# Kernel optimization log

Measured on AMD Instinct MI355X. Metric: run time of the kernel, lower is better.

The kernel has to match this reference:

```python
import jax, jax.numpy as jnp
import numpy as np

B, N, D, H = 16, 256, 1024, 8
DK = D // H
WAVE_LEN = 1000.0


def box_relational_embedding(boxes):
    # boxes: (B, N, 4) as (x_min, y_min, x_max, y_max)
    x_min, y_min, x_max, y_max = jnp.split(boxes, 4, axis=-1)  # each (B, N, 1)
    cx = (x_min + x_max) * 0.5
    cy = (y_min + y_max) * 0.5
    w = (x_max - x_min) + 1.0
    h = (y_max - y_min) + 1.0
    # pairwise deltas (B, N, N); row i = query box, col j = key box
    delta_x = jnp.log(jnp.clip(jnp.abs((cx - jnp.swapaxes(cx, -2, -1)) / w), 1e-3, None))
    delta_y = jnp.log(jnp.clip(jnp.abs((cy - jnp.swapaxes(cy, -2, -1)) / h), 1e-3, None))
    delta_w = jnp.log(w / jnp.swapaxes(w, -2, -1))
    delta_h = jnp.log(h / jnp.swapaxes(h, -2, -1))
    pos = jnp.stack([delta_x, delta_y, delta_w, delta_h], axis=-1)  # (B, N, N, 4)
    # sinusoidal expansion: dim_g = 64 -> 8 frequencies per delta
    feat_range = jnp.arange(8, dtype=pos.dtype) / 8.0
    dim_mat = 1.0 / (WAVE_LEN ** feat_range)  # (8,)
    mul = (100.0 * pos)[..., None] * dim_mat  # (B, N, N, 4, 8)
    mul = mul.reshape(pos.shape[:3] + (32,))
    return jnp.concatenate([jnp.sin(mul), jnp.cos(mul)], axis=-1)  # (B, N, N, 64)


def setup_inputs() -> dict:
    key = jax.random.key(0)
    ks = jax.random.split(key, 12)
    x = jax.random.normal(ks[0], (B, N, D), dtype=jnp.float32)
    # valid boxes: x_max > x_min, y_max > y_min
    xy = jax.random.uniform(ks[1], (B, N, 2), dtype=jnp.float32) * 100.0
    wh = jax.random.uniform(ks[2], (B, N, 2), dtype=jnp.float32) * 50.0 + 1.0
    boxes = jnp.concatenate([xy, xy + wh], axis=-1)
    s = 1.0 / np.sqrt(D)
    Wq = jax.random.normal(ks[3], (D, D), dtype=jnp.float32) * s
    Wk = jax.random.normal(ks[4], (D, D), dtype=jnp.float32) * s
    Wv = jax.random.normal(ks[5], (D, D), dtype=jnp.float32) * s
    Wo = jax.random.normal(ks[6], (D, D), dtype=jnp.float32) * s
    bq = jnp.zeros((D,), jnp.float32)
    bk = jnp.zeros((D,), jnp.float32)
    bv = jnp.zeros((D,), jnp.float32)
    bo = jnp.zeros((D,), jnp.float32)
    Wg = jax.random.normal(ks[7], (H, 64), dtype=jnp.float32) * (1.0 / 8.0)  # 8 per-head (64->1) linears
    bg = jnp.zeros((H,), jnp.float32)
    return {"x": x, "boxes": boxes, "Wq": Wq, "bq": bq, "Wk": Wk, "bk": bk,
            "Wv": Wv, "bv": bv, "Wo": Wo, "bo": bo, "Wg": Wg, "bg": bg}


def reference(x, boxes, Wq, bq, Wk, bk, Wv, bv, Wo, bo, Wg, bg):
    emb = box_relational_embedding(boxes)  # (B, N, N, 64)
    # per-head geometric weights, ReLU'd: (B, H, N, N)
    geo = jax.nn.relu(jnp.einsum('bnmg,hg->bhnm', emb, Wg) + bg[None, :, None, None])
    q = (x @ Wq + bq).reshape(B, N, H, DK).transpose(0, 2, 1, 3)  # (B, H, N, DK)
    k = (x @ Wk + bk).reshape(B, N, H, DK).transpose(0, 2, 1, 3)
    v = (x @ Wv + bv).reshape(B, N, H, DK).transpose(0, 2, 1, 3)
    scores = jnp.einsum('bhnd,bhmd->bhnm', q, k) / np.sqrt(DK)
    w_mn = jax.nn.softmax(jnp.log(jnp.clip(geo, 1e-6, None)) + scores, axis=-1)
    out = jnp.einsum('bhnm,bhmd->bhnd', w_mn, v)  # (B, H, N, DK)
    out = out.transpose(0, 2, 1, 3).reshape(B, N, D)
    return out @ Wo + bo
```

## Files before the change

kernel.cpp:

```cpp
#include <hip/hip_runtime.h>
#include <hip/hip_fp16.h>

#define Bb 16
#define Nn 256
#define Dd 1024
#define Hh 8
#define DKk 128

typedef unsigned short u16;
typedef __attribute__((ext_vector_type(8))) short bfrag;
typedef __attribute__((ext_vector_type(4))) float f4;

#define MFMA16(a, b, c) __builtin_amdgcn_mfma_f32_16x16x32_bf16((a), (b), (c), 0, 0, 0)

__device__ __forceinline__ u16 f2b(float f) {
  unsigned int u = __builtin_bit_cast(unsigned int, f);
  u += 0x7fffu + ((u >> 16) & 1u);
  return (u16)(u >> 16);
}

typedef __attribute__((address_space(1))) void GV;
typedef __attribute__((address_space(3))) void LV;
__device__ __forceinline__ void gload16(const void* g, void* l) {
  __builtin_amdgcn_global_load_lds((GV*)g, (LV*)l, 16, 0, 0);
}

__global__ __launch_bounds__(256) void cast_x_kernel(const float* __restrict__ x,
                                                     u16* __restrict__ xb) {
  const int i = blockIdx.x * 256 + threadIdx.x;
  const float4 v = ((const float4*)x)[i];
  union { u16 u[4]; unsigned long long ll; } p;
  p.u[0] = f2b(v.x); p.u[1] = f2b(v.y); p.u[2] = f2b(v.z); p.u[3] = f2b(v.w);
  ((unsigned long long*)xb)[i] = p.ll;
}

__global__ __launch_bounds__(256) void transpose_w_kernel(
    const float* __restrict__ Wq, const float* __restrict__ Wk,
    const float* __restrict__ Wv, const float* __restrict__ Wo,
    u16* __restrict__ wqkvt, u16* __restrict__ wot) {
  __shared__ float t[32][33];
  const int bid = blockIdx.x;
  const int which = bid >> 10;
  const int tr = (bid >> 5) & 31;
  const int tc = bid & 31;
  const float* W = which == 0 ? Wq : which == 1 ? Wk : which == 2 ? Wv : Wo;
  u16* dst = (which == 3) ? wot : (wqkvt + (long long)which * 1024 * 1024);
  const int tx = threadIdx.x & 31, ty = threadIdx.x >> 5;
#pragma unroll
  for (int rr = 0; rr < 4; rr++)
    t[ty + rr * 8][tx] = W[(tr * 32 + ty + rr * 8) * 1024 + tc * 32 + tx];
  __syncthreads();
#pragma unroll
  for (int rr = 0; rr < 4; rr++)
    dst[(tc * 32 + ty + rr * 8) * 1024 + tr * 32 + tx] = f2b(t[tx][ty + rr * 8]);
}

__global__ __launch_bounds__(256) void transpose_v_kernel(const u16* __restrict__ v,
                                                          u16* __restrict__ vT) {
  __shared__ u16 t[32][33];
  const int bid = blockIdx.x;
  const int bh = bid >> 5;
  const int kt = (bid >> 2) & 7;
  const int ct = bid & 3;
  const u16* src = v + (long long)bh * Nn * DKk;
  u16* dst = vT + (long long)bh * DKk * Nn;
  const int tx = threadIdx.x & 31, ty = threadIdx.x >> 5;
#pragma unroll
  for (int rr = 0; rr < 4; rr++)
    t[ty + rr * 8][tx] = src[(kt * 32 + ty + rr * 8) * DKk + ct * 32 + tx];
  __syncthreads();
#pragma unroll
  for (int rr = 0; rr < 4; rr++)
    dst[(ct * 32 + ty + rr * 8) * Nn + kt * 32 + tx] = t[tx][ty + rr * 8];
}

__global__ __launch_bounds__(256) void geo_kernel(const float* __restrict__ boxes,
                                                  const float* __restrict__ Wg,
                                                  const float* __restrict__ bg,
                                                  __half* __restrict__ logg) {
  __shared__ float wg_s[512];
  __shared__ float bg_s[8];
  const int tid = threadIdx.x;
  wg_s[tid] = Wg[tid];
  wg_s[tid + 256] = Wg[tid + 256];
  if (tid < 8) bg_s[tid] = bg[tid];
  __syncthreads();
  const int bid = blockIdx.x;
  const int b = bid >> 8, i = bid & 255;
  const int j = tid;
  const float4 bi4 = ((const float4*)boxes)[b * 256 + i];
  const float4 bj4 = ((const float4*)boxes)[b * 256 + j];
  const float cxi = (bi4.x + bi4.z) * 0.5f, cyi = (bi4.y + bi4.w) * 0.5f;
  const float wi = bi4.z - bi4.x + 1.f, hi = bi4.w - bi4.y + 1.f;
  const float cxj = (bj4.x + bj4.z) * 0.5f, cyj = (bj4.y + bj4.w) * 0.5f;
  const float wj = bj4.z - bj4.x + 1.f, hj = bj4.w - bj4.y + 1.f;
  float pos[4];
  pos[0] = __logf(fmaxf(fabsf((cxi - cxj) / wi), 1e-3f));
  pos[1] = __logf(fmaxf(fabsf((cyi - cyj) / hi), 1e-3f));
  pos[2] = __logf(wi / wj);
  pos[3] = __logf(hi / hj);
  const float dimm[8] = {1.0f, 0.42169650342f, 0.177827941f, 0.0749894209f,
                         0.0316227766f, 0.01333521432f, 0.00562341325f, 0.00237137371f};
  float sv[32], cv[32];
#pragma unroll
  for (int d = 0; d < 4; d++)
#pragma unroll
    for (int f = 0; f < 8; f++) {
      const float ang = 100.f * pos[d] * dimm[f];
      __sincosf(ang, &sv[d * 8 + f], &cv[d * 8 + f]);
    }
  const long long base = ((long long)(b * 8) * 256 + i) * 256 + j;
#pragma unroll
  for (int h = 0; h < 8; h++) {
    float a = bg_s[h];
#pragma unroll
    for (int t = 0; t < 32; t++)
      a = fmaf(sv[t], wg_s[h * 64 + t], fmaf(cv[t], wg_s[h * 64 + 32 + t], a));
    logg[base + (long long)h * 65536] = __float2half(__logf(fmaxf(a, 1e-6f)));
  }
}

template <int MODE>
__global__ __launch_bounds__(256) void gemm128(
    const u16* __restrict__ A, const u16* __restrict__ Bt,
    const float* __restrict__ b0, const float* __restrict__ b1,
    const float* __restrict__ b2, u16* __restrict__ oq, u16* __restrict__ ok,
    u16* __restrict__ ov, float* __restrict__ co, int M, int Np, int K) {
  __shared__ u16 As[128 * 32];
  __shared__ u16 Bs[128 * 32];
  const int tilesN = Np >> 7;
  const int bm = blockIdx.x / tilesN, bn = blockIdx.x - bm * tilesN;
  const int m0 = bm << 7, n0 = bn << 7;
  const int tid = threadIdx.x, lane = tid & 63, w = tid >> 6;
  const int wr = w >> 1, wc = w & 1;
  const int fr = lane & 15, fq = lane >> 4;

  f4 acc[4][4];
#pragma unroll
  for (int i = 0; i < 4; i++)
#pragma unroll
    for (int j = 0; j < 4; j++) acc[i][j] = (f4){0.f, 0.f, 0.f, 0.f};

  const int srow = (w << 5) + (lane >> 2);
  const int skel = (lane & 3) << 3;
  const u16* Ag0 = A + (long long)(m0 + srow) * K + skel;
  const u16* Ag1 = Ag0 + 16 * K;
  const u16* Bg0 = Bt + (long long)(n0 + srow) * K + skel;
  const u16* Bg1 = Bg0 + 16 * K;
  u16* Al0 = As + (w << 5) * 32;
  u16* Al1 = Al0 + 16 * 32;
  u16* Bl0 = Bs + (w << 5) * 32;
  u16* Bl1 = Bl0 + 16 * 32;

  for (int k0 = 0; k0 < K; k0 += 32) {
    __syncthreads();
    gload16(Ag0 + k0, Al0);
    gload16(Ag1 + k0, Al1);
    gload16(Bg0 + k0, Bl0);
    gload16(Bg1 + k0, Bl1);
    __syncthreads();
    bfrag av[4], bv[4];
#pragma unroll
    for (int i = 0; i < 4; i++)
      av[i] = *(const bfrag*)(As + ((wr << 6) + (i << 4) + fr) * 32 + (fq << 3));
#pragma unroll
    for (int j = 0; j < 4; j++)
      bv[j] = *(const bfrag*)(Bs + ((wc << 6) + (j << 4) + fr) * 32 + (fq << 3));
#pragma unroll
    for (int i = 0; i < 4; i++)
#pragma unroll
      for (int j = 0; j < 4; j++) acc[i][j] = MFMA16(av[i], bv[j], acc[i][j]);
  }

  if constexpr (MODE == 0) {
#pragma unroll
    for (int j = 0; j < 4; j++) {
      const int n = n0 + (wc << 6) + (j << 4) + fr;
      const int which = n >> 10;
      const int hh = (n >> 7) & 7;
      const int dk = n & 127;
      const float bia = (which == 0 ? b0 : which == 1 ? b1 : b2)[n & 1023];
      u16* dst = (which == 0 ? oq : which == 1 ? ok : ov);
      const float scl = (which == 0) ? 0.08838834764831845f : 1.0f;
#pragma unroll
      for (int i = 0; i < 4; i++)
#pragma unroll
        for (int r = 0; r < 4; r++) {
          const int m = m0 + (wr << 6) + (i << 4) + (fq << 2) + r;
          const int bidx = m >> 8, itok = m & 255;
          dst[((long long)(bidx * 8 + hh) * 256 + itok) * 128 + dk] =
              f2b((acc[i][j][r] + bia) * scl);
        }
    }
  } else {
#pragma unroll
    for (int i = 0; i < 4; i++)
#pragma unroll
      for (int j = 0; j < 4; j++) {
        const int n = n0 + (wc << 6) + (j << 4) + fr;
        const float bia = b0[n];
#pragma unroll
        for (int r = 0; r < 4; r++) {
          const int m = m0 + (wr << 6) + (i << 4) + (fq << 2) + r;
          co[(long long)m * Np + n] = acc[i][j][r] + bia;
        }
      }
  }
}

__global__ __launch_bounds__(256, 4) void attn_kernel(
    const u16* __restrict__ q, const u16* __restrict__ k,
    const u16* __restrict__ vT, const __half* __restrict__ logg,
    u16* __restrict__ aout) {
  __shared__ __align__(16) char smem[16384 + 17408 + 256];
  __half* ggs = (__half*)smem;
  u16* plds = (u16*)(smem + 16384);
  float* mbuf = (float*)(smem + 16384);
  float* mlb = (float*)(smem + 16384 + 17408);

  const int bid = blockIdx.x;
  const int qt = bid & 7;
  const int bh = bid >> 3;
  const int tid = threadIdx.x, lane = tid & 63, w = tid >> 6;
  const int rg = w >> 1, kh = w & 1;
  const int fr = lane & 15, fq = lane >> 4;
  const int i0 = qt * 32 + rg * 16;

  const u16* qp = q + (long long)bh * Nn * DKk;
  const u16* kp = k + (long long)bh * Nn * DKk + kh * 128 * DKk;
  const u16* vp = vT + (long long)bh * DKk * Nn;
  const __half* gp = logg + (long long)bh * Nn * Nn;

  __half* ggw = ggs + w * (16 * 128);
  {
    const int r4 = lane >> 4, c8 = lane & 15;
#pragma unroll
    for (int t = 0; t < 4; t++)
      gload16(gp + (i0 + t * 4 + r4) * Nn + kh * 128 + c8 * 8, ggw + t * 512);
  }

  bfrag qf[4];
#pragma unroll
  for (int ks = 0; ks < 4; ks++)
    qf[ks] = *(const bfrag*)(qp + (i0 + fr) * DKk + ks * 32 + fq * 8);

  f4 s[8];
#pragma unroll
  for (int j = 0; j < 8; j++) s[j] = (f4){0.f, 0.f, 0.f, 0.f};
#pragma unroll
  for (int j = 0; j < 8; j++)
#pragma unroll
    for (int ks = 0; ks < 4; ks++) {
      bfrag kf = *(const bfrag*)(kp + (j * 16 + fr) * DKk + ks * 32 + fq * 8);
      s[j] = MFMA16(qf[ks], kf, s[j]);
    }

  asm volatile("s_waitcnt vmcnt(0)" ::: "memory");

#pragma unroll
  for (int j = 0; j < 8; j++)
#pragma unroll
    for (int r = 0; r < 4; r++)
      s[j][r] += __half2float(ggw[(fq * 4 + r) * 128 + j * 16 + fr]);

  float mr[4], lr[4];
#pragma unroll
  for (int r = 0; r < 4; r++) {
    float m = s[0][r];
#pragma unroll
    for (int j = 1; j < 8; j++) m = fmaxf(m, s[j][r]);
    m = fmaxf(m, __shfl_xor(m, 1));
    m = fmaxf(m, __shfl_xor(m, 2));
    m = fmaxf(m, __shfl_xor(m, 4));
    m = fmaxf(m, __shfl_xor(m, 8));
    float t = 0.f;
#pragma unroll
    for (int j = 0; j < 8; j++) {
      const float p = __expf(s[j][r] - m);
      s[j][r] = p;
      t += p;
    }
    t += __shfl_xor(t, 1);
    t += __shfl_xor(t, 2);
    t += __shfl_xor(t, 4);
    t += __shfl_xor(t, 8);
    mr[r] = m;
    lr[r] = t;
  }

  u16* pw = plds + w * (16 * 136);
#pragma unroll
  for (int j = 0; j < 8; j++)
#pragma unroll
    for (int r = 0; r < 4; r++)
      pw[(fq * 4 + r) * 136 + j * 16 + fr] = f2b(s[j][r]);
  __syncthreads();

  f4 o[8];
#pragma unroll
  for (int d = 0; d < 8; d++) o[d] = (f4){0.f, 0.f, 0.f, 0.f};
#pragma unroll
  for (int jt = 0; jt < 4; jt++) {
    bfrag pf = *(const bfrag*)(pw + fr * 136 + jt * 32 + fq * 8);
#pragma unroll
    for (int d = 0; d < 8; d++) {
      bfrag vf = *(const bfrag*)(vp + (d * 16 + fr) * Nn + kh * 128 + jt * 32 + fq * 8);
      o[d] = MFMA16(pf, vf, o[d]);
    }
  }
  __syncthreads();

  if (kh) {
    float* ob = mbuf + rg * (16 * 132);
#pragma unroll
    for (int d = 0; d < 8; d++)
#pragma unroll
      for (int r = 0; r < 4; r++)
        ob[(fq * 4 + r) * 132 + d * 16 + fr] = o[d][r];
    if (fr == 0)
#pragma unroll
      for (int r = 0; r < 4; r++) {
        mlb[rg * 32 + (fq * 4 + r) * 2] = mr[r];
        mlb[rg * 32 + (fq * 4 + r) * 2 + 1] = lr[r];
      }
  }
  __syncthreads();

  if (!kh) {
    const int b = bh >> 3, h = bh & 7;
    float a0[4], a1[4], invl[4];
#pragma unroll
    for (int r = 0; r < 4; r++) {
      const float m1 = mlb[rg * 32 + (fq * 4 + r) * 2];
      const float l1 = mlb[rg * 32 + (fq * 4 + r) * 2 + 1];
      const float m = fmaxf(mr[r], m1);
      a0[r] = __expf(mr[r] - m);
      a1[r] = __expf(m1 - m);
      invl[r] = 1.0f / (lr[r] * a0[r] + l1 * a1[r]);
    }
    const float* ob = mbuf + rg * (16 * 132);
#pragma unroll
    for (int d = 0; d < 8; d++)
#pragma unroll
      for (int r = 0; r < 4; r++) {
        const float o1 = ob[(fq * 4 + r) * 132 + d * 16 + fr];
        const float val = (o[d][r] * a0[r] + o1 * a1[r]) * invl[r];
        const int row = i0 + fq * 4 + r;
        const int dk = d * 16 + fr;
        aout[((long long)(b * 256 + row)) * 1024 + h * 128 + dk] = f2b(val);
      }
  }
}

extern "C" void kernel_launch(void* const* d_in, const int* in_sizes, int n_in,
                              void* d_out, int out_size, void* d_ws, size_t ws_size,
                              hipStream_t stream) {
  (void)in_sizes; (void)n_in; (void)out_size; (void)ws_size;
  const float* x = (const float*)d_in[0];
  const float* boxes = (const float*)d_in[1];
  const float* Wq = (const float*)d_in[2];
  const float* bq = (const float*)d_in[3];
  const float* Wk = (const float*)d_in[4];
  const float* bk = (const float*)d_in[5];
  const float* Wv = (const float*)d_in[6];
  const float* bv = (const float*)d_in[7];
  const float* Wo = (const float*)d_in[8];
  const float* bo = (const float*)d_in[9];
  const float* Wg = (const float*)d_in[10];
  const float* bg = (const float*)d_in[11];
  float* out = (float*)d_out;

  char* ws = (char*)d_ws;
  u16* xb    = (u16*)(ws);
  u16* wqkvt = (u16*)(ws + (8ll << 20));
  u16* wot   = (u16*)(ws + (14ll << 20));
  u16* qb    = (u16*)(ws + (16ll << 20));
  u16* kb    = (u16*)(ws + (24ll << 20));
  u16* vb    = (u16*)(ws + (32ll << 20));
  u16* vtb   = (u16*)(ws + (40ll << 20));
  __half* logg = (__half*)(ws + (48ll << 20));
  u16* aout  = (u16*)(ws + (64ll << 20));

  cast_x_kernel<<<4096, 256, 0, stream>>>(x, xb);
  transpose_w_kernel<<<4096, 256, 0, stream>>>(Wq, Wk, Wv, Wo, wqkvt, wot);
  geo_kernel<<<4096, 256, 0, stream>>>(boxes, Wg, bg, logg);
  gemm128<0><<<32 * 24, 256, 0, stream>>>(xb, wqkvt, bq, bk, bv, qb, kb, vb,
                                          nullptr, 4096, 3072, 1024);
  transpose_v_kernel<<<4096, 256, 0, stream>>>(vb, vtb);
  attn_kernel<<<1024, 256, 0, stream>>>(qb, kb, vtb, logg, aout);
  gemm128<1><<<32 * 8, 256, 0, stream>>>(aout, wot, bo, nullptr, nullptr, nullptr,
                                         nullptr, nullptr, out, 4096, 1024, 1024);
}
```

Before: 233.9 us.

## Replace QKV GEMM with 256x256 double-buffered, swizzled, interleaved-load MFMA kernel

Replaces the 128x128 single-buffered QKV projection GEMM with a 256x256-tile, 512-thread kernel. It uses double-buffered LDS with a K-step of 64, an XOR-swizzled LDS layout, and asynchronous global-to-LDS loads for the next tile issued between MFMA quadrants, with s_setprio raised around the compute. It also remaps block IDs for locality. The aim is to hide global load latency and cut LDS bank conflicts in the largest GEMM. In exchange it needs more LDS and registers, allows one block per CU, and launches only 192 blocks.

```diff
diff --git a/kernel.cpp b/kernel.cpp
--- a/kernel.cpp
+++ b/kernel.cpp
@@ -120,12 +120,140 @@
   }
 }
 
-template <int MODE>
-__global__ __launch_bounds__(256) void gemm128(
+#define LDA_SUB(AV, ihalf)                                                      \
+  _Pragma("unroll") for (int i_ = 0; i_ < 4; i_++) {                            \
+    const int row_ = wm * 128 + (ihalf) * 64 + i_ * 16 + fr;                    \
+    AV[i_][0] = *(const bfrag*)(Asc + row_ * 64 + acol0);                       \
+    AV[i_][1] = *(const bfrag*)(Asc + row_ * 64 + acol1);                       \
+  }
+#define LDB_SUB(BV, jhalf)                                                      \
+  _Pragma("unroll") for (int j_ = 0; j_ < 2; j_++) {                            \
+    const int row_ = wn * 64 + (jhalf) * 32 + j_ * 16 + fr;                     \
+    BV[j_][0] = *(const bfrag*)(Bsc + row_ * 64 + acol0);                       \
+    BV[j_][1] = *(const bfrag*)(Bsc + row_ * 64 + acol1);                       \
+  }
+#define QUAD(I0, J0, AV, BV)                                                    \
+  _Pragma("unroll") for (int i_ = 0; i_ < 4; i_++)                              \
+  _Pragma("unroll") for (int j_ = 0; j_ < 2; j_++)                              \
+  _Pragma("unroll") for (int ks_ = 0; ks_ < 2; ks_++)                           \
+    acc[(I0) + i_][(J0) + j_] =                                                 \
+        MFMA16(AV[i_][ks_], BV[j_][ks_], acc[(I0) + i_][(J0) + j_]);
+#define STG_A(kt_, r_, dA) \
+  gload16(Agp + (long long)(r_) * 65536 + (kt_) * 64, (dA) + (r_) * 4096 + (w << 9))
+#define STG_B(kt_, r_, dB) \
+  gload16(Bgp + (long long)(r_) * 65536 + (kt_) * 64, (dB) + (r_) * 4096 + (w << 9))
+#define BAR() __builtin_amdgcn_s_barrier()
+#define PRIO1() __builtin_amdgcn_s_setprio(1)
+#define PRIO0() __builtin_amdgcn_s_setprio(0)
+
+__global__ __launch_bounds__(512, 1) void gemm256_qkv(
     const u16* __restrict__ A, const u16* __restrict__ Bt,
     const float* __restrict__ b0, const float* __restrict__ b1,
     const float* __restrict__ b2, u16* __restrict__ oq, u16* __restrict__ ok,
-    u16* __restrict__ ov, float* __restrict__ co, int M, int Np, int K) {
+    u16* __restrict__ ov) {
+  __shared__ u16 AsF[2 * 16384];
+  __shared__ u16 BsF[2 * 16384];
+  const int tid = threadIdx.x, lane = tid & 63, w = tid >> 6;
+  const int wm = w >> 2, wn = w & 3;
+  const int fr = lane & 15, fq = lane >> 4;
+
+  const int bid = (blockIdx.x & 7) * 24 + (blockIdx.x >> 3);
+  const int bm = bid / 12, bn = bid - bm * 12;
+  const int m0 = bm << 8, n0 = bn << 8;
+
+  const int acol0 = (fq * 8) ^ ((fr & 7) * 8);
+  const int acol1 = (32 + fq * 8) ^ ((fr & 7) * 8);
+
+  const int srw = tid >> 3;
+  const int scol = (((tid & 7) ^ (srw & 7)) << 3);
+  const u16* Agp = A + (long long)(m0 + srw) * 1024 + scol;
+  const u16* Bgp = Bt + (long long)(n0 + srw) * 1024 + scol;
+
+  f4 acc[8][4];
+#pragma unroll
+  for (int i = 0; i < 8; i++)
+#pragma unroll
+    for (int j = 0; j < 4; j++) acc[i][j] = (f4){0.f, 0.f, 0.f, 0.f};
+
+  {
+    u16* dA = AsF; u16* dB = BsF;
+    STG_A(0, 0, dA); STG_A(0, 2, dA);
+    STG_B(0, 0, dB); STG_B(0, 1, dB); STG_B(0, 2, dB); STG_B(0, 3, dB);
+    STG_A(0, 1, dA); STG_A(0, 3, dA);
+  }
+
+  bfrag aV[4][2], b0V[2][2], b1V[2][2];
+
+  for (int kt = 0; kt < 15; ++kt) {
+    const int cur = kt & 1;
+    const u16* Asc = AsF + cur * 16384;
+    const u16* Bsc = BsF + cur * 16384;
+    u16* dA = AsF + (cur ^ 1) * 16384;
+    u16* dB = BsF + (cur ^ 1) * 16384;
+    asm volatile("s_waitcnt vmcnt(2)" ::: "memory");
+    BAR();
+    LDA_SUB(aV, 0); LDB_SUB(b0V, 0);
+    STG_A(kt + 1, 0, dA); STG_A(kt + 1, 2, dA);
+    BAR();
+    PRIO1(); QUAD(0, 0, aV, b0V); PRIO0();
+    BAR();
+    LDB_SUB(b1V, 1);
+    STG_B(kt + 1, 0, dB); STG_B(kt + 1, 1, dB);
+    BAR();
+    PRIO1(); QUAD(0, 2, aV, b1V); PRIO0();
+    BAR();
+    asm volatile("s_waitcnt vmcnt(4)" ::: "memory");
+    BAR();
+    LDA_SUB(aV, 1);
+    STG_B(kt + 1, 2, dB); STG_B(kt + 1, 3, dB);
+    BAR();
+    PRIO1(); QUAD(4, 2, aV, b1V); PRIO0();
+    BAR();
+    STG_A(kt + 1, 1, dA); STG_A(kt + 1, 3, dA);
+    BAR();
+    PRIO1(); QUAD(4, 0, aV, b0V); PRIO0();
+    BAR();
+  }
+  {
+    const u16* Asc = AsF + 16384;
+    const u16* Bsc = BsF + 16384;
+    asm volatile("s_waitcnt vmcnt(2)" ::: "memory");
+    BAR();
+    LDA_SUB(aV, 0); LDB_SUB(b0V, 0);
+    PRIO1(); QUAD(0, 0, aV, b0V); PRIO0();
+    LDB_SUB(b1V, 1);
+    PRIO1(); QUAD(0, 2, aV, b1V); PRIO0();
+    asm volatile("s_waitcnt vmcnt(0)" ::: "memory");
+    BAR();
+    LDA_SUB(aV, 1);
+    QUAD(4, 2, aV, b1V);
+    QUAD(4, 0, aV, b0V);
+  }
+
+#pragma unroll
+  for (int j = 0; j < 4; j++) {
+    const int n = n0 + wn * 64 + j * 16 + fr;
+    const int which = n >> 10;
+    const int hh = (n >> 7) & 7;
+    const int dk = n & 127;
+    const float bia = (which == 0 ? b0 : which == 1 ? b1 : b2)[n & 1023];
+    u16* dst = (which == 0 ? oq : which == 1 ? ok : ov);
+    const float scl = (which == 0) ? 0.08838834764831845f : 1.0f;
+#pragma unroll
+    for (int i = 0; i < 8; i++)
+#pragma unroll
+      for (int r = 0; r < 4; r++) {
+        const int m = m0 + wm * 128 + i * 16 + fq * 4 + r;
+        const int bidx = m >> 8, itok = m & 255;
+        dst[((long long)(bidx * 8 + hh) * 256 + itok) * 128 + dk] =
+            f2b((acc[i][j][r] + bia) * scl);
+      }
+  }
+}
+
+__global__ __launch_bounds__(256) void gemm128_out(
+    const u16* __restrict__ A, const u16* __restrict__ Bt,
+    const float* __restrict__ b0, float* __restrict__ co, int Np, int K) {
   __shared__ u16 As[128 * 32];
   __shared__ u16 Bs[128 * 32];
   const int tilesN = Np >> 7;
@@ -172,40 +300,18 @@
       for (int j = 0; j < 4; j++) acc[i][j] = MFMA16(av[i], bv[j], acc[i][j]);
   }
 
-  if constexpr (MODE == 0) {
+#pragma unroll
+  for (int i = 0; i < 4; i++)
 #pragma unroll
     for (int j = 0; j < 4; j++) {
       const int n = n0 + (wc << 6) + (j << 4) + fr;
-      const int which = n >> 10;
-      const int hh = (n >> 7) & 7;
-      const int dk = n & 127;
-      const float bia = (which == 0 ? b0 : which == 1 ? b1 : b2)[n & 1023];
-      u16* dst = (which == 0 ? oq : which == 1 ? ok : ov);
-      const float scl = (which == 0) ? 0.08838834764831845f : 1.0f;
-#pragma unroll
-      for (int i = 0; i < 4; i++)
-#pragma unroll
-        for (int r = 0; r < 4; r++) {
-          const int m = m0 + (wr << 6) + (i << 4) + (fq << 2) + r;
-          const int bidx = m >> 8, itok = m & 255;
-          dst[((long long)(bidx * 8 + hh) * 256 + itok) * 128 + dk] =
-              f2b((acc[i][j][r] + bia) * scl);
-        }
-    }
-  } else {
-#pragma unroll
-    for (int i = 0; i < 4; i++)
-#pragma unroll
-      for (int j = 0; j < 4; j++) {
-        const int n = n0 + (wc << 6) + (j << 4) + fr;
-        const float bia = b0[n];
-#pragma unroll
-        for (int r = 0; r < 4; r++) {
-          const int m = m0 + (wr << 6) + (i << 4) + (fq << 2) + r;
-          co[(long long)m * Np + n] = acc[i][j][r] + bia;
-        }
+      const float bia = b0[n];
+#pragma unroll
+      for (int r = 0; r < 4; r++) {
+        const int m = m0 + (wr << 6) + (i << 4) + (fq << 2) + r;
+        co[(long long)m * Np + n] = acc[i][j][r] + bia;
       }
-  }
+    }
 }
 
 __global__ __launch_bounds__(256, 4) void attn_kernel(
@@ -384,10 +490,8 @@
   cast_x_kernel<<<4096, 256, 0, stream>>>(x, xb);
   transpose_w_kernel<<<4096, 256, 0, stream>>>(Wq, Wk, Wv, Wo, wqkvt, wot);
   geo_kernel<<<4096, 256, 0, stream>>>(boxes, Wg, bg, logg);
-  gemm128<0><<<32 * 24, 256, 0, stream>>>(xb, wqkvt, bq, bk, bv, qb, kb, vb,
-                                          nullptr, 4096, 3072, 1024);
+  gemm256_qkv<<<192, 512, 0, stream>>>(xb, wqkvt, bq, bk, bv, qb, kb, vb);
   transpose_v_kernel<<<4096, 256, 0, stream>>>(vb, vtb);
   attn_kernel<<<1024, 256, 0, stream>>>(qb, kb, vtb, logg, aout);
-  gemm128<1><<<32 * 8, 256, 0, stream>>>(aout, wot, bo, nullptr, nullptr, nullptr,
-                                         nullptr, nullptr, out, 4096, 1024, 1024);
-}
+  gemm128_out<<<32 * 8, 256, 0, stream>>>(aout, wot, bo, out, 1024, 1024);
+}
```

Result: faster. 229.1 us (-2.1%).
